# Performance work log

Hardware: AMD Instinct MI355X
Metric: run time of the kernel (lower is better)

Reference implementation:

```python
import jax, jax.numpy as jnp
import numpy as np

D_MODEL = 1024
N_HEADS = 16
HEAD_DIM = D_MODEL // N_HEADS
B, T = 4, 2048


def setup_inputs() -> dict:
    key = jax.random.key(0)
    ks = jax.random.split(key, 5)
    s = 0.02
    return {
        "x": jax.random.normal(ks[0], (B, T, D_MODEL), dtype=jnp.float32),
        "w_qkv": jax.random.normal(ks[1], (D_MODEL, 3 * D_MODEL), dtype=jnp.float32) * s,
        "b_qkv": jnp.zeros((3 * D_MODEL,), dtype=jnp.float32),
        "w_out": jax.random.normal(ks[2], (D_MODEL, D_MODEL), dtype=jnp.float32) * s,
        "b_out": jnp.zeros((D_MODEL,), dtype=jnp.float32),
    }


def reference(x, w_qkv, b_qkv, w_out, b_out):
    Bx, Tx, C = x.shape
    H, Dh = N_HEADS, HEAD_DIM
    qkv = x @ w_qkv + b_qkv                      # [B,T,3C]
    qkv = qkv.reshape(Bx, Tx, 3, H, Dh)
    q = jnp.transpose(qkv[:, :, 0], (0, 2, 1, 3))  # [B,H,T,Dh]
    k = jnp.transpose(qkv[:, :, 1], (0, 2, 1, 3))
    v = jnp.transpose(qkv[:, :, 2], (0, 2, 1, 3))
    scale = 1.0 / jnp.sqrt(jnp.asarray(Dh, dtype=x.dtype))
    attn = jnp.einsum("bhqd,bhkd->bhqk", q, k) * scale  # [B,H,T,T]
    causal = jnp.tril(jnp.ones((Tx, Tx), dtype=bool))
    attn = jnp.where(causal, attn, jnp.asarray(-jnp.inf, dtype=attn.dtype))
    attn = jax.nn.softmax(attn, axis=-1)
    out = jnp.einsum("bhqk,bhkd->bhqd", attn, v)  # [B,H,T,Dh]
    out = jnp.transpose(out, (0, 2, 1, 3)).reshape(Bx, Tx, C)
    return out @ w_out + b_out
```

## Files before the change

kernel.cpp:

```cpp
#include <hip/hip_runtime.h>
#include <hip/hip_bf16.h>
#include <stdint.h>

#define DM    1024
#define NH    16
#define DH    64
#define BATCH 4
#define SEQ   2048
#define QSCALE 0.18033688011112042f

typedef __attribute__((ext_vector_type(4))) float f32x4;
typedef __attribute__((ext_vector_type(8))) short short8;

__device__ __forceinline__ void async_load16(const void* g, void* l) {
    __builtin_amdgcn_global_load_lds(
        (const __attribute__((address_space(1))) void*)(uintptr_t)g,
        (__attribute__((address_space(3))) void*)(uintptr_t)l,
        16, 0, 0);
}

__global__ __launch_bounds__(256) void k_convert(const float* __restrict__ in,
                                                 __hip_bfloat16* __restrict__ out,
                                                 int n4, int* __restrict__ cnt) {
    if (blockIdx.x == 0 && threadIdx.x == 0) cnt[0] = 0;
    int i = blockIdx.x * 256 + threadIdx.x;
    if (i >= n4) return;
    float4 v = ((const float4*)in)[i];
    union { ushort4 u; __hip_bfloat16 h[4]; } o;
    o.h[0] = __float2bfloat16(v.x);
    o.h[1] = __float2bfloat16(v.y);
    o.h[2] = __float2bfloat16(v.z);
    o.h[3] = __float2bfloat16(v.w);
    ((ushort4*)out)[i] = o.u;
}

__global__ __launch_bounds__(256) void k_transpose(const float* __restrict__ in,
                                                   __hip_bfloat16* __restrict__ out,
                                                   int K, int N) {
    __shared__ float tile[32][33];
    const int n0 = blockIdx.x * 32, k0 = blockIdx.y * 32;
    const int tx = threadIdx.x, ty = threadIdx.y;
#pragma unroll
    for (int i = 0; i < 32; i += 8)
        tile[ty + i][tx] = in[(size_t)(k0 + ty + i) * N + n0 + tx];
    __syncthreads();
#pragma unroll
    for (int i = 0; i < 32; i += 8)
        out[(size_t)(n0 + ty + i) * K + k0 + tx] = __float2bfloat16(tile[tx][ty + i]);
}

__global__ __launch_bounds__(256) void k_gemm_qkv(
    const __hip_bfloat16* __restrict__ A, const __hip_bfloat16* __restrict__ Bt,
    const float* __restrict__ bias,
    __hip_bfloat16* __restrict__ qo, __hip_bfloat16* __restrict__ ko,
    __hip_bfloat16* __restrict__ vto) {
    constexpr int K = 1024;
    __shared__ __align__(16) __hip_bfloat16 As[128 * 64];
    __shared__ __align__(16) __hip_bfloat16 Bs[128 * 64];
    const int tid = threadIdx.x;
    const int lane = tid & 63, wid = tid >> 6;
    const int quad = lane >> 4, c = lane & 15;
    const int m0 = blockIdx.y * 128, n0 = blockIdx.x * 128;
    const int wm = (wid & 1) * 64, wn = (wid >> 1) * 64;
    f32x4 acc[4][4] = {};

    for (int k0 = 0; k0 < K; k0 += 64) {
        __syncthreads();
#pragma unroll
        for (int i = 0; i < 4; ++i) {
            const int s = tid + i * 256;
            const int r = s >> 3;
            const int g = (s & 7) ^ (r & 7);
            async_load16(A  + (size_t)(m0 + r) * K + k0 + g * 8, As + s * 8);
            async_load16(Bt + (size_t)(n0 + r) * K + k0 + g * 8, Bs + s * 8);
        }
        __syncthreads();
#pragma unroll
        for (int kk = 0; kk < 2; ++kk) {
            short8 af[4], bf[4];
#pragma unroll
            for (int mt = 0; mt < 4; ++mt) {
                const int R = wm + mt * 16 + c;
                af[mt] = *(const short8*)(As + R * 64 + (((kk * 4 + quad) ^ (R & 7)) * 8));
            }
#pragma unroll
            for (int nt = 0; nt < 4; ++nt) {
                const int R = wn + nt * 16 + c;
                bf[nt] = *(const short8*)(Bs + R * 64 + (((kk * 4 + quad) ^ (R & 7)) * 8));
            }
#pragma unroll
            for (int mt = 0; mt < 4; ++mt)
#pragma unroll
                for (int nt = 0; nt < 4; ++nt)
                    acc[mt][nt] = __builtin_amdgcn_mfma_f32_16x16x32_bf16(
                        af[mt], bf[nt], acc[mt][nt], 0, 0, 0);
        }
    }

    const int sel = n0 >> 10;
#pragma unroll
    for (int mt = 0; mt < 4; ++mt) {
        const int t0m = m0 + wm + mt * 16 + quad * 4;
        const int b = t0m >> 11, t0 = t0m & 2047;
#pragma unroll
        for (int nt = 0; nt < 4; ++nt) {
            const int n = n0 + wn + nt * 16 + c;
            const int h = (n & 1023) >> 6, dh = n & 63;
            const int bh = b * 16 + h;
            const float bv = bias[n];
            if (sel == 0) {
#pragma unroll
                for (int r = 0; r < 4; ++r)
                    qo[((size_t)bh * 2048 + t0 + r) * 64 + dh] =
                        __float2bfloat16((acc[mt][nt][r] + bv) * QSCALE);
            } else if (sel == 1) {
#pragma unroll
                for (int r = 0; r < 4; ++r)
                    ko[((size_t)bh * 2048 + t0 + r) * 64 + dh] =
                        __float2bfloat16(acc[mt][nt][r] + bv);
            } else {
                union { ushort4 u; __hip_bfloat16 hh[4]; } pk;
#pragma unroll
                for (int r = 0; r < 4; ++r)
                    pk.hh[r] = __float2bfloat16(acc[mt][nt][r] + bv);
                *(ushort4*)(vto + ((size_t)bh * 64 + dh) * 2048 + t0) = pk.u;
            }
        }
    }
}

__global__ __launch_bounds__(256) void k_attn(
    const __hip_bfloat16* __restrict__ q, const __hip_bfloat16* __restrict__ k,
    const __hip_bfloat16* __restrict__ vt, __hip_bfloat16* __restrict__ y,
    int* __restrict__ cnt) {
    __shared__ __align__(16) __hip_bfloat16 Ks[2][64 * 64];
    __shared__ __align__(16) __hip_bfloat16 Vts[2][64 * 64];
    __shared__ int s_item;
    const int tid = threadIdx.x;
    const int lane = tid & 63, w = tid >> 6;
    const int quad = lane >> 4, c = lane & 15;
    const short one = (short)0x3F80;
    const short8 ones = {one, one, one, one, one, one, one, one};

    for (;;) {
        __syncthreads();
        if (tid == 0) s_item = atomicAdd(cnt, 1);
        __syncthreads();
        const int item = s_item;
        if (item >= 1024) break;
        const int qt = 15 - (item >> 6);
        const int bh = item & 63;
        const int b = bh >> 4, h = bh & 15;
        const int q0 = qt * 128;
        const int qw = q0 + w * 32;
        const int nkt = 2 * qt + 2;
        const size_t kbase0 = (size_t)bh * 2048 * 64;
        const size_t vbase0 = (size_t)bh * 64 * 2048;

        short8 qf[2][2];
#pragma unroll
        for (int j = 0; j < 2; ++j) {
            const __hip_bfloat16* qrow = q + ((size_t)bh * 2048 + qw + j * 16 + c) * 64;
            qf[0][j] = *(const short8*)(qrow + quad * 8);
            qf[1][j] = *(const short8*)(qrow + 32 + quad * 8);
        }

        f32x4 accO[2][4] = {};
        f32x4 accL[2] = {};

        auto stage = [&](int kt, int buf) {
#pragma unroll
            for (int i = 0; i < 2; ++i) {
                const int s = tid + i * 256;
                const int r = s >> 3;
                const int g = (s & 7) ^ (r & 7);
                async_load16(k  + kbase0 + (size_t)(kt * 64 + r) * 64 + g * 8,
                             &Ks[buf][s * 8]);
                async_load16(vt + vbase0 + (size_t)r * 2048 + kt * 64 + g * 8,
                             &Vts[buf][s * 8]);
            }
        };

        stage(0, 0);
        for (int kt = 0; kt < nkt; ++kt) {
            const int buf = kt & 1;
            __syncthreads();
            if (kt + 1 < nkt) stage(kt + 1, buf ^ 1);
            if (kt * 64 > qw + 31) continue;
            const __hip_bfloat16* Kb = Ks[buf];
            const __hip_bfloat16* Vb = Vts[buf];

            short8 kf[4][2];
#pragma unroll
            for (int nt = 0; nt < 4; ++nt) {
                const __hip_bfloat16* kr = Kb + (nt * 16 + c) * 64;
                kf[nt][0] = *(const short8*)(kr + ((quad ^ (c & 7)) * 8));
                kf[nt][1] = *(const short8*)(kr + (((quad + 4) ^ (c & 7)) * 8));
            }

            short8 pf[2][2];
#pragma unroll
            for (int j = 0; j < 2; ++j) {
                f32x4 sj[4];
                __builtin_amdgcn_s_setprio(1);
#pragma unroll
                for (int nt = 0; nt < 4; ++nt) {
                    f32x4 z = {};
                    z      = __builtin_amdgcn_mfma_f32_16x16x32_bf16(kf[nt][0], qf[0][j], z, 0, 0, 0);
                    sj[nt] = __builtin_amdgcn_mfma_f32_16x16x32_bf16(kf[nt][1], qf[1][j], z, 0, 0, 0);
                }
                __builtin_amdgcn_s_setprio(0);
                if (kt * 64 + 63 > qw + j * 16) {
                    const int qg = qw + j * 16 + c;
#pragma unroll
                    for (int nt = 0; nt < 4; ++nt) {
                        const int keyb = kt * 64 + nt * 16 + quad * 4;
#pragma unroll
                        for (int r = 0; r < 4; ++r)
                            if (keyb + r > qg) sj[nt][r] = -1e30f;
                    }
                }
#pragma unroll
                for (int nt = 0; nt < 4; ++nt)
#pragma unroll
                    for (int r = 0; r < 4; ++r)
                        sj[nt][r] = __builtin_amdgcn_exp2f(sj[nt][r]);
                unsigned pk32[4][2];
#pragma unroll
                for (int nt = 0; nt < 4; ++nt) {
                    asm("v_cvt_pk_bf16_f32 %0, %1, %2"
                        : "=v"(pk32[nt][0]) : "v"(sj[nt][0]), "v"(sj[nt][1]));
                    asm("v_cvt_pk_bf16_f32 %0, %1, %2"
                        : "=v"(pk32[nt][1]) : "v"(sj[nt][2]), "v"(sj[nt][3]));
                }
                union U8 { unsigned u[4]; short8 v; } w0, w1;
#pragma unroll
                for (int rr = 0; rr < 2; ++rr) {
                    auto t1 = __builtin_amdgcn_permlane32_swap(pk32[0][rr], pk32[1][rr], false, false);
                    auto t2 = __builtin_amdgcn_permlane16_swap(t1[0], t1[1], false, false);
                    w0.u[rr]     = t2[0];
                    w0.u[2 + rr] = t2[1];
                    t1 = __builtin_amdgcn_permlane32_swap(pk32[2][rr], pk32[3][rr], false, false);
                    t2 = __builtin_amdgcn_permlane16_swap(t1[0], t1[1], false, false);
                    w1.u[rr]     = t2[0];
                    w1.u[2 + rr] = t2[1];
                }
                pf[0][j] = w0.v;
                pf[1][j] = w1.v;
            }

            __builtin_amdgcn_s_setprio(1);
#pragma unroll
            for (int j = 0; j < 2; ++j) {
                accL[j] = __builtin_amdgcn_mfma_f32_16x16x32_bf16(ones, pf[0][j], accL[j], 0, 0, 0);
                accL[j] = __builtin_amdgcn_mfma_f32_16x16x32_bf16(ones, pf[1][j], accL[j], 0, 0, 0);
            }
#pragma unroll
            for (int dt = 0; dt < 4; ++dt) {
                const __hip_bfloat16* vr = Vb + (dt * 16 + c) * 64;
                short8 vf0 = *(const short8*)(vr + ((quad ^ (c & 7)) * 8));
                short8 vf1 = *(const short8*)(vr + (((quad + 4) ^ (c & 7)) * 8));
#pragma unroll
                for (int j = 0; j < 2; ++j) {
                    accO[j][dt] = __builtin_amdgcn_mfma_f32_16x16x32_bf16(vf0, pf[0][j], accO[j][dt], 0, 0, 0);
                    accO[j][dt] = __builtin_amdgcn_mfma_f32_16x16x32_bf16(vf1, pf[1][j], accO[j][dt], 0, 0, 0);
                }
            }
            __builtin_amdgcn_s_setprio(0);
        }
#pragma unroll
        for (int j = 0; j < 2; ++j) {
            const float inv = 1.0f / accL[j][0];
            const int qg = qw + j * 16 + c;
#pragma unroll
            for (int dt = 0; dt < 4; ++dt) {
                union { ushort4 u; __hip_bfloat16 hh[4]; } o;
#pragma unroll
                for (int r = 0; r < 4; ++r)
                    o.hh[r] = __float2bfloat16(accO[j][dt][r] * inv);
                *(ushort4*)(y + ((size_t)b * 2048 + qg) * 1024 + h * 64 + dt * 16 + quad * 4) = o.u;
            }
        }
    }
}

__global__ __launch_bounds__(256) void k_gemm_out(
    const __hip_bfloat16* __restrict__ A, const __hip_bfloat16* __restrict__ Bt,
    const float* __restrict__ bias, float* __restrict__ out) {
    constexpr int K = 1024;
    __shared__ __align__(16) __hip_bfloat16 As[128 * 64];
    __shared__ __align__(16) __hip_bfloat16 Bs[128 * 64];
    const int tid = threadIdx.x;
    const int lane = tid & 63, wid = tid >> 6;
    const int quad = lane >> 4, c = lane & 15;
    const int m0 = blockIdx.y * 128, n0 = blockIdx.x * 128;
    const int wm = (wid & 1) * 64, wn = (wid >> 1) * 64;
    f32x4 acc[4][4] = {};

    for (int k0 = 0; k0 < K; k0 += 64) {
        __syncthreads();
#pragma unroll
        for (int i = 0; i < 4; ++i) {
            const int s = tid + i * 256;
            const int r = s >> 3;
            const int g = (s & 7) ^ (r & 7);
            async_load16(A  + (size_t)(m0 + r) * K + k0 + g * 8, As + s * 8);
            async_load16(Bt + (size_t)(n0 + r) * K + k0 + g * 8, Bs + s * 8);
        }
        __syncthreads();
#pragma unroll
        for (int kk = 0; kk < 2; ++kk) {
            short8 af[4], bf[4];
#pragma unroll
            for (int mt = 0; mt < 4; ++mt) {
                const int R = wm + mt * 16 + c;
                af[mt] = *(const short8*)(As + R * 64 + (((kk * 4 + quad) ^ (R & 7)) * 8));
            }
#pragma unroll
            for (int nt = 0; nt < 4; ++nt) {
                const int R = wn + nt * 16 + c;
                bf[nt] = *(const short8*)(Bs + R * 64 + (((kk * 4 + quad) ^ (R & 7)) * 8));
            }
#pragma unroll
            for (int mt = 0; mt < 4; ++mt)
#pragma unroll
                for (int nt = 0; nt < 4; ++nt)
                    acc[mt][nt] = __builtin_amdgcn_mfma_f32_16x16x32_bf16(
                        af[mt], bf[nt], acc[mt][nt], 0, 0, 0);
        }
    }
#pragma unroll
    for (int mt = 0; mt < 4; ++mt) {
        const int m = m0 + wm + mt * 16 + quad * 4;
#pragma unroll
        for (int nt = 0; nt < 4; ++nt) {
            const int n = n0 + wn + nt * 16 + c;
            const float bv = bias[n];
#pragma unroll
            for (int r = 0; r < 4; ++r)
                out[(size_t)(m + r) * 1024 + n] = acc[mt][nt][r] + bv;
        }
    }
}

extern "C" void kernel_launch(void* const* d_in, const int* in_sizes, int n_in,
                              void* d_out, int out_size, void* d_ws, size_t ws_size,
                              hipStream_t stream) {
    (void)in_sizes; (void)n_in; (void)out_size; (void)ws_size;
    const float* x     = (const float*)d_in[0];
    const float* w_qkv = (const float*)d_in[1];
    const float* b_qkv = (const float*)d_in[2];
    const float* w_out = (const float*)d_in[3];
    const float* b_out = (const float*)d_in[4];
    float* out = (float*)d_out;

    char* ws = (char*)d_ws;
    __hip_bfloat16* xb    = (__hip_bfloat16*)(ws + 0);
    __hip_bfloat16* wqkvT = (__hip_bfloat16*)(ws + 16777216);
    __hip_bfloat16* woutT = (__hip_bfloat16*)(ws + 23068672);
    __hip_bfloat16* qb    = (__hip_bfloat16*)(ws + 25165824);
    __hip_bfloat16* kb    = (__hip_bfloat16*)(ws + 41943040);
    __hip_bfloat16* vtb   = (__hip_bfloat16*)(ws + 58720256);
    __hip_bfloat16* yb    = (__hip_bfloat16*)(ws + 75497472);

    int* cnt = (int*)d_out;

    k_convert<<<8192, 256, 0, stream>>>(x, xb, 2097152, cnt);
    k_transpose<<<dim3(96, 32), dim3(32, 8), 0, stream>>>(w_qkv, wqkvT, 1024, 3072);
    k_transpose<<<dim3(32, 32), dim3(32, 8), 0, stream>>>(w_out, woutT, 1024, 1024);
    k_gemm_qkv<<<dim3(24, 64), 256, 0, stream>>>(xb, wqkvT, b_qkv, qb, kb, vtb);
    k_attn<<<dim3(1024), 256, 0, stream>>>(qb, kb, vtb, yb, cnt);
    k_gemm_out<<<dim3(8, 64), 256, 0, stream>>>(yb, woutT, b_out, out);
}
```

Measured before the change: 255.0 us.

## Widen GEMM tiles to 128x256 with 8 waves and overlap next-tile loads

Both projection GEMMs move from 128x128 tiles with 4 waves to 128x256 tiles with 8 waves. Each iteration now reads its fragments into registers first, then issues the async global-to-LDS loads for the next K slice, and runs the MFMAs at raised priority. The goal is to hide global load latency behind compute and to reuse each A tile across more columns. The cost is fewer blocks: 256 for the output GEMM, which may leave some of the MI355X's compute units underused.

```diff
diff --git a/kernel.cpp b/kernel.cpp
--- a/kernel.cpp
+++ b/kernel.cpp
@@ -49,52 +49,71 @@
         out[(size_t)(n0 + ty + i) * K + k0 + tx] = __float2bfloat16(tile[tx][ty + i]);
 }
 
-__global__ __launch_bounds__(256) void k_gemm_qkv(
+__global__ __launch_bounds__(512) void k_gemm_qkv(
     const __hip_bfloat16* __restrict__ A, const __hip_bfloat16* __restrict__ Bt,
     const float* __restrict__ bias,
     __hip_bfloat16* __restrict__ qo, __hip_bfloat16* __restrict__ ko,
     __hip_bfloat16* __restrict__ vto) {
     constexpr int K = 1024;
+    constexpr int NT = K / 64;
     __shared__ __align__(16) __hip_bfloat16 As[128 * 64];
-    __shared__ __align__(16) __hip_bfloat16 Bs[128 * 64];
+    __shared__ __align__(16) __hip_bfloat16 Bs[256 * 64];
     const int tid = threadIdx.x;
     const int lane = tid & 63, wid = tid >> 6;
     const int quad = lane >> 4, c = lane & 15;
-    const int m0 = blockIdx.y * 128, n0 = blockIdx.x * 128;
-    const int wm = (wid & 1) * 64, wn = (wid >> 1) * 64;
+    const int m0 = blockIdx.y * 128, n0 = blockIdx.x * 256;
+    const int wm = (wid >> 2) * 64, wn = (wid & 3) * 64;
     f32x4 acc[4][4] = {};
 
-    for (int k0 = 0; k0 < K; k0 += 64) {
-        __syncthreads();
-#pragma unroll
-        for (int i = 0; i < 4; ++i) {
-            const int s = tid + i * 256;
+    auto stage = [&](int k0) {
+#pragma unroll
+        for (int i = 0; i < 2; ++i) {
+            const int s = tid + i * 512;
             const int r = s >> 3;
             const int g = (s & 7) ^ (r & 7);
-            async_load16(A  + (size_t)(m0 + r) * K + k0 + g * 8, As + s * 8);
+            async_load16(A + (size_t)(m0 + r) * K + k0 + g * 8, As + s * 8);
+        }
+#pragma unroll
+        for (int i = 0; i < 4; ++i) {
+            const int s = tid + i * 512;
+            const int r = s >> 3;
+            const int g = (s & 7) ^ (r & 7);
             async_load16(Bt + (size_t)(n0 + r) * K + k0 + g * 8, Bs + s * 8);
         }
-        __syncthreads();
-#pragma unroll
-        for (int kk = 0; kk < 2; ++kk) {
-            short8 af[4], bf[4];
-#pragma unroll
-            for (int mt = 0; mt < 4; ++mt) {
-                const int R = wm + mt * 16 + c;
-                af[mt] = *(const short8*)(As + R * 64 + (((kk * 4 + quad) ^ (R & 7)) * 8));
-            }
-#pragma unroll
-            for (int nt = 0; nt < 4; ++nt) {
-                const int R = wn + nt * 16 + c;
-                bf[nt] = *(const short8*)(Bs + R * 64 + (((kk * 4 + quad) ^ (R & 7)) * 8));
-            }
+    };
+
+    stage(0);
+    for (int t = 0; t < NT; ++t) {
+        asm volatile("s_waitcnt vmcnt(0)" ::: "memory");
+        __builtin_amdgcn_s_barrier();
+        short8 af[4][2], bf[4][2];
+#pragma unroll
+        for (int mt = 0; mt < 4; ++mt) {
+            const int R = wm + mt * 16 + c;
+#pragma unroll
+            for (int kk = 0; kk < 2; ++kk)
+                af[mt][kk] = *(const short8*)(As + R * 64 + (((kk * 4 + quad) ^ (R & 7)) * 8));
+        }
+#pragma unroll
+        for (int nt = 0; nt < 4; ++nt) {
+            const int R = wn + nt * 16 + c;
+#pragma unroll
+            for (int kk = 0; kk < 2; ++kk)
+                bf[nt][kk] = *(const short8*)(Bs + R * 64 + (((kk * 4 + quad) ^ (R & 7)) * 8));
+        }
+        asm volatile("s_waitcnt lgkmcnt(0)" ::: "memory");
+        __builtin_amdgcn_s_barrier();
+        if (t + 1 < NT) stage((t + 1) * 64);
+        __builtin_amdgcn_s_setprio(1);
+#pragma unroll
+        for (int kk = 0; kk < 2; ++kk)
 #pragma unroll
             for (int mt = 0; mt < 4; ++mt)
 #pragma unroll
                 for (int nt = 0; nt < 4; ++nt)
                     acc[mt][nt] = __builtin_amdgcn_mfma_f32_16x16x32_bf16(
-                        af[mt], bf[nt], acc[mt][nt], 0, 0, 0);
-        }
+                        af[mt][kk], bf[nt][kk], acc[mt][nt], 0, 0, 0);
+        __builtin_amdgcn_s_setprio(0);
     }
 
     const int sel = n0 >> 10;
@@ -284,50 +303,69 @@
     }
 }
 
-__global__ __launch_bounds__(256) void k_gemm_out(
+__global__ __launch_bounds__(512) void k_gemm_out(
     const __hip_bfloat16* __restrict__ A, const __hip_bfloat16* __restrict__ Bt,
     const float* __restrict__ bias, float* __restrict__ out) {
     constexpr int K = 1024;
+    constexpr int NT = K / 64;
     __shared__ __align__(16) __hip_bfloat16 As[128 * 64];
-    __shared__ __align__(16) __hip_bfloat16 Bs[128 * 64];
+    __shared__ __align__(16) __hip_bfloat16 Bs[256 * 64];
     const int tid = threadIdx.x;
     const int lane = tid & 63, wid = tid >> 6;
     const int quad = lane >> 4, c = lane & 15;
-    const int m0 = blockIdx.y * 128, n0 = blockIdx.x * 128;
-    const int wm = (wid & 1) * 64, wn = (wid >> 1) * 64;
+    const int m0 = blockIdx.y * 128, n0 = blockIdx.x * 256;
+    const int wm = (wid >> 2) * 64, wn = (wid & 3) * 64;
     f32x4 acc[4][4] = {};
 
-    for (int k0 = 0; k0 < K; k0 += 64) {
-        __syncthreads();
-#pragma unroll
-        for (int i = 0; i < 4; ++i) {
-            const int s = tid + i * 256;
+    auto stage = [&](int k0) {
+#pragma unroll
+        for (int i = 0; i < 2; ++i) {
+            const int s = tid + i * 512;
             const int r = s >> 3;
             const int g = (s & 7) ^ (r & 7);
-            async_load16(A  + (size_t)(m0 + r) * K + k0 + g * 8, As + s * 8);
+            async_load16(A + (size_t)(m0 + r) * K + k0 + g * 8, As + s * 8);
+        }
+#pragma unroll
+        for (int i = 0; i < 4; ++i) {
+            const int s = tid + i * 512;
+            const int r = s >> 3;
+            const int g = (s & 7) ^ (r & 7);
             async_load16(Bt + (size_t)(n0 + r) * K + k0 + g * 8, Bs + s * 8);
         }
-        __syncthreads();
-#pragma unroll
-        for (int kk = 0; kk < 2; ++kk) {
-            short8 af[4], bf[4];
-#pragma unroll
-            for (int mt = 0; mt < 4; ++mt) {
-                const int R = wm + mt * 16 + c;
-                af[mt] = *(const short8*)(As + R * 64 + (((kk * 4 + quad) ^ (R & 7)) * 8));
-            }
-#pragma unroll
-            for (int nt = 0; nt < 4; ++nt) {
-                const int R = wn + nt * 16 + c;
-                bf[nt] = *(const short8*)(Bs + R * 64 + (((kk * 4 + quad) ^ (R & 7)) * 8));
-            }
+    };
+
+    stage(0);
+    for (int t = 0; t < NT; ++t) {
+        asm volatile("s_waitcnt vmcnt(0)" ::: "memory");
+        __builtin_amdgcn_s_barrier();
+        short8 af[4][2], bf[4][2];
+#pragma unroll
+        for (int mt = 0; mt < 4; ++mt) {
+            const int R = wm + mt * 16 + c;
+#pragma unroll
+            for (int kk = 0; kk < 2; ++kk)
+                af[mt][kk] = *(const short8*)(As + R * 64 + (((kk * 4 + quad) ^ (R & 7)) * 8));
+        }
+#pragma unroll
+        for (int nt = 0; nt < 4; ++nt) {
+            const int R = wn + nt * 16 + c;
+#pragma unroll
+            for (int kk = 0; kk < 2; ++kk)
+                bf[nt][kk] = *(const short8*)(Bs + R * 64 + (((kk * 4 + quad) ^ (R & 7)) * 8));
+        }
+        asm volatile("s_waitcnt lgkmcnt(0)" ::: "memory");
+        __builtin_amdgcn_s_barrier();
+        if (t + 1 < NT) stage((t + 1) * 64);
+        __builtin_amdgcn_s_setprio(1);
+#pragma unroll
+        for (int kk = 0; kk < 2; ++kk)
 #pragma unroll
             for (int mt = 0; mt < 4; ++mt)
 #pragma unroll
                 for (int nt = 0; nt < 4; ++nt)
                     acc[mt][nt] = __builtin_amdgcn_mfma_f32_16x16x32_bf16(
-                        af[mt], bf[nt], acc[mt][nt], 0, 0, 0);
-        }
+                        af[mt][kk], bf[nt][kk], acc[mt][nt], 0, 0, 0);
+        __builtin_amdgcn_s_setprio(0);
     }
 #pragma unroll
     for (int mt = 0; mt < 4; ++mt) {
@@ -368,7 +406,7 @@
     k_convert<<<8192, 256, 0, stream>>>(x, xb, 2097152, cnt);
     k_transpose<<<dim3(96, 32), dim3(32, 8), 0, stream>>>(w_qkv, wqkvT, 1024, 3072);
     k_transpose<<<dim3(32, 32), dim3(32, 8), 0, stream>>>(w_out, woutT, 1024, 1024);
-    k_gemm_qkv<<<dim3(24, 64), 256, 0, stream>>>(xb, wqkvT, b_qkv, qb, kb, vtb);
+    k_gemm_qkv<<<dim3(12, 64), 512, 0, stream>>>(xb, wqkvT, b_qkv, qb, kb, vtb);
     k_attn<<<dim3(1024), 256, 0, stream>>>(qb, kb, vtb, yb, cnt);
-    k_gemm_out<<<dim3(8, 64), 256, 0, stream>>>(yb, woutT, b_out, out);
-}
+    k_gemm_out<<<dim3(4, 64), 512, 0, stream>>>(yb, woutT, b_out, out);
+}
```

Result: no change. 251.9 us (-1.2%).
